# Performance work log

Hardware: AMD Instinct MI355X
Metric: run time of the kernel (lower is better)

## Reference

```python
import jax, jax.numpy as jnp
import numpy as np

B, T, D = 2, 2048, 2048
N_HEADS, N_KV = 16, 4
HD = D // N_HEADS  # 128
ROPE_BASE = 10000.0


def _rope_tables(t, dim, base=ROPE_BASE):
    inv_freq = 1.0 / (base ** (jnp.arange(0, dim, 2, dtype=jnp.float32) / dim))
    freqs = jnp.arange(t, dtype=jnp.float32)[:, None] * inv_freq[None, :]  # (T, dim/2)
    emb = jnp.concatenate([freqs, freqs], axis=-1)  # (T, dim)
    return jnp.cos(emb), jnp.sin(emb)


def _rotate_half(x):
    x1, x2 = jnp.split(x, 2, axis=-1)
    return jnp.concatenate([-x2, x1], axis=-1)


def _apply_rope(x, cos, sin):
    # x: (B, H, T, hd); cos/sin: (T, hd)
    return x * cos[None, None] + _rotate_half(x) * sin[None, None]


def setup_inputs() -> dict:
    key = jax.random.key(0)
    ks = jax.random.split(key, 5)
    s = 0.02
    return {
        "x": jax.random.normal(ks[0], (B, T, D), jnp.float32),
        "wq": jax.random.normal(ks[1], (D, N_HEADS * HD), jnp.float32) * s,
        "wk": jax.random.normal(ks[2], (D, N_KV * HD), jnp.float32) * s,
        "wv": jax.random.normal(ks[3], (D, N_KV * HD), jnp.float32) * s,
        "wo": jax.random.normal(ks[4], (D, D), jnp.float32) * s,
    }


def reference(x, wq, wk, wv, wo):
    b, t, c = x.shape
    n_rep = N_HEADS // N_KV
    scale = 1.0 / np.sqrt(HD)

    q = (x @ wq).reshape(b, t, N_HEADS, HD).transpose(0, 2, 1, 3)  # (B,H,T,hd)
    k = (x @ wk).reshape(b, t, N_KV, HD).transpose(0, 2, 1, 3)     # (B,Hkv,T,hd)
    v = (x @ wv).reshape(b, t, N_KV, HD).transpose(0, 2, 1, 3)

    cos, sin = _rope_tables(t, HD)
    q = _apply_rope(q, cos, sin)
    k = _apply_rope(k, cos, sin)

    # repeat_kv (GQA)
    k = jnp.repeat(k, n_rep, axis=1)  # (B,H,T,hd)
    v = jnp.repeat(v, n_rep, axis=1)

    scores = jnp.einsum("bhqd,bhkd->bhqk", q, k) * scale
    causal = jnp.tril(jnp.ones((t, t), dtype=bool))
    scores = jnp.where(causal[None, None], scores, -jnp.inf)
    attn = jax.nn.softmax(scores, axis=-1)
    out = jnp.einsum("bhqk,bhkd->bhqd", attn, v)
    out = out.transpose(0, 2, 1, 3).reshape(b, t, c)
    return out @ wo
```

## Files before the change

### kernel.cpp

```cpp
#include <hip/hip_runtime.h>
#include <hip/hip_bf16.h>
#include <math.h>

#define B_   2
#define T_   2048
#define D_   2048
#define NH_  16
#define NKV_ 4
#define HD_  128
#define MROWS (B_*T_)
#define NQKV  (NH_*HD_ + 2*NKV_*HD_)

typedef __bf16 bf16_t;
typedef __bf16 bf16x8 __attribute__((ext_vector_type(8)));
typedef __bf16 bf16x4 __attribute__((ext_vector_type(4)));
typedef float  floatx4 __attribute__((ext_vector_type(4)));

__device__ __forceinline__ void async_copy16(const bf16_t* gsrc, bf16_t* ldst) {
  __builtin_amdgcn_global_load_lds(
      (const __attribute__((address_space(1))) unsigned int*)gsrc,
      (__attribute__((address_space(3))) unsigned int*)ldst, 16, 0, 0);
}

__global__ void cast_f32_bf16(const float* __restrict__ src, bf16_t* __restrict__ dst, int n) {
  int i = (blockIdx.x * 256 + threadIdx.x) * 8;
  if (i >= n) return;
  float4 a = *(const float4*)(src + i);
  float4 b = *(const float4*)(src + i + 4);
  bf16x8 v;
  v[0]=(bf16_t)a.x; v[1]=(bf16_t)a.y; v[2]=(bf16_t)a.z; v[3]=(bf16_t)a.w;
  v[4]=(bf16_t)b.x; v[5]=(bf16_t)b.y; v[6]=(bf16_t)b.z; v[7]=(bf16_t)b.w;
  *(bf16x8*)(dst + i) = v;
}

__global__ void transpose_cast4(const float* __restrict__ s0, const float* __restrict__ s1,
                                const float* __restrict__ s2, const float* __restrict__ s3,
                                bf16_t* __restrict__ d0, bf16_t* __restrict__ d1,
                                bf16_t* __restrict__ d2, bf16_t* __restrict__ d3) {
  const int z = blockIdx.z;
  const int N = (z == 1 || z == 2) ? 512 : 2048;
  const int n0 = blockIdx.x * 32;
  if (n0 >= N) return;
  const float* src = (z == 0) ? s0 : (z == 1) ? s1 : (z == 2) ? s2 : s3;
  bf16_t*      dst = (z == 0) ? d0 : (z == 1) ? d1 : (z == 2) ? d2 : d3;
  const int K = 2048;
  __shared__ float tile[32][33];
  int k0 = blockIdx.y * 32;
  int tx = threadIdx.x, ty = threadIdx.y;
#pragma unroll
  for (int r = 0; r < 4; r++)
    tile[ty + r*8][tx] = src[(size_t)(k0 + ty + r*8) * N + n0 + tx];
  __syncthreads();
#pragma unroll
  for (int r = 0; r < 4; r++)
    dst[(size_t)(n0 + ty + r*8) * K + k0 + tx] = (bf16_t)tile[tx][ty + r*8];
}

template <typename OUT_T>
__global__ __launch_bounds__(256, 2)
void gemm_bt(const bf16_t* __restrict__ A, const bf16_t* __restrict__ Bt,
             OUT_T* __restrict__ C, int M, int N, int K) {
  __shared__ __align__(16) bf16_t As[128 * 64];
  __shared__ __align__(16) bf16_t Bs[128 * 64];
  const int tid  = threadIdx.x;
  const int wave = tid >> 6, lane = tid & 63;
  const int quad = lane >> 4, l16 = lane & 15;
  const int nBlocksM = M >> 7;
  const int bm = blockIdx.x % nBlocksM, bn = blockIdx.x / nBlocksM;
  const int m0 = bm * 128, n0 = bn * 128;
  const int wm = (wave >> 1) * 64, wn = (wave & 1) * 64;

  floatx4 acc[4][4];
#pragma unroll
  for (int i = 0; i < 4; i++)
#pragma unroll
    for (int j = 0; j < 4; j++) acc[i][j] = floatx4{0.f, 0.f, 0.f, 0.f};

  for (int k0 = 0; k0 < K; k0 += 64) {
    __syncthreads();
#pragma unroll
    for (int i = 0; i < 4; i++) {
      int e = i * 256 + tid;
      int row = e >> 3, grp = e & 7;
      int gg = grp ^ (row & 7);
      async_copy16(A + (size_t)(m0 + row) * K + k0 + gg * 8, As + e * 8);
    }
#pragma unroll
    for (int i = 0; i < 4; i++) {
      int e = i * 256 + tid;
      int row = e >> 3, grp = e & 7;
      int gg = grp ^ (row & 7);
      async_copy16(Bt + (size_t)(n0 + row) * K + k0 + gg * 8, Bs + e * 8);
    }
    __syncthreads();
#pragma unroll
    for (int ks = 0; ks < 2; ks++) {
      bf16x8 af[4], bfr[4];
      int grp = ks * 4 + quad;
#pragma unroll
      for (int mi = 0; mi < 4; mi++) {
        int row = wm + mi * 16 + l16;
        af[mi] = *(const bf16x8*)(As + row * 64 + ((grp ^ (row & 7)) << 3));
      }
#pragma unroll
      for (int ni = 0; ni < 4; ni++) {
        int row = wn + ni * 16 + l16;
        bfr[ni] = *(const bf16x8*)(Bs + row * 64 + ((grp ^ (row & 7)) << 3));
      }
#pragma unroll
      for (int mi = 0; mi < 4; mi++)
#pragma unroll
        for (int ni = 0; ni < 4; ni++)
          acc[mi][ni] = __builtin_amdgcn_mfma_f32_16x16x32_bf16(af[mi], bfr[ni], acc[mi][ni], 0, 0, 0);
    }
  }
#pragma unroll
  for (int mi = 0; mi < 4; mi++) {
#pragma unroll
    for (int r = 0; r < 4; r++) {
      int row = m0 + wm + mi * 16 + quad * 4 + r;
      size_t base = (size_t)row * N + n0 + wn;
#pragma unroll
      for (int ni = 0; ni < 4; ni++)
        C[base + ni * 16 + l16] = (OUT_T)acc[mi][ni][r];
    }
  }
}

__global__ void rope_scatter(const bf16_t* __restrict__ qkv,
                             bf16_t* __restrict__ Qb, bf16_t* __restrict__ Kb) {
  int g = blockIdx.x * 256 + threadIdx.x;
  int j = g & 63;
  int rest = g >> 6;
  int head = rest % (NH_ + NKV_);
  int row  = rest / (NH_ + NKV_);
  int t = row & (T_ - 1);
  int b = row >> 11;
  const bf16_t* src = qkv + (size_t)row * NQKV;
  float ang = (float)t * __expf(-0.14391156816f * (float)j);
  float sn, cs;
  __sincosf(ang, &sn, &cs);
  if (head < NH_) {
    float x0 = (float)src[head * HD_ + j];
    float x1 = (float)src[head * HD_ + 64 + j];
    const float scale = 0.12751651541057752f;
    bf16_t* dst = Qb + ((size_t)(b * NH_ + head) * T_ + t) * HD_;
    dst[j]      = (bf16_t)((x0 * cs - x1 * sn) * scale);
    dst[j + 64] = (bf16_t)((x1 * cs + x0 * sn) * scale);
  } else {
    int kvh = head - NH_;
    float x0 = (float)src[NH_ * HD_ + kvh * HD_ + j];
    float x1 = (float)src[NH_ * HD_ + kvh * HD_ + 64 + j];
    bf16_t* dst = Kb + ((size_t)(b * NKV_ + kvh) * T_ + t) * HD_;
    dst[j]      = (bf16_t)(x0 * cs - x1 * sn);
    dst[j + 64] = (bf16_t)(x1 * cs + x0 * sn);
  }
}

__global__ void v_transpose(const bf16_t* __restrict__ qkv, bf16_t* __restrict__ Vt) {
  __shared__ float tile[32][33];
  int t0 = blockIdx.x * 32, d0 = blockIdx.y * 32;
  int bk = blockIdx.z;
  int b = bk / NKV_, kvh = bk % NKV_;
  int tx = threadIdx.x, ty = threadIdx.y;
#pragma unroll
  for (int r = 0; r < 4; r++) {
    int t = t0 + ty + r * 8;
    tile[ty + r*8][tx] =
        (float)qkv[(size_t)(b * T_ + t) * NQKV + (NH_ + NKV_) * HD_ + kvh * HD_ + d0 + tx];
  }
  __syncthreads();
#pragma unroll
  for (int r = 0; r < 4; r++) {
    int d = d0 + ty + r * 8;
    Vt[((size_t)(b * NKV_ + kvh) * HD_ + d) * T_ + t0 + tx] = (bf16_t)tile[tx][ty + r*8];
  }
}

__global__ __launch_bounds__(256, 2)
void flash_attn(const bf16_t* __restrict__ Qb, const bf16_t* __restrict__ Kb,
                const bf16_t* __restrict__ Vt, bf16_t* __restrict__ Ob) {
  __shared__ __align__(16) bf16_t Ks[2][64 * 128];
  __shared__ __align__(16) bf16_t Vs[2][128 * 64];
  __shared__ __align__(16) bf16_t Ps[4][16 * 72];

  const int tid = threadIdx.x;
  const int wave = tid >> 6, lane = tid & 63;
  const int quad = lane >> 4, l16 = lane & 15;
  const int nQT = T_ / 64;
  const int bid = blockIdx.x;
  const int bh = bid % (B_ * NH_);
  const int qt = (nQT - 1) - (bid / (B_ * NH_));
  const int h = bh % NH_;
  const int b = bh / NH_;
  const int kv = h >> 2;

  const bf16_t* qbase = Qb + ((size_t)(b * NH_ + h) * T_ + qt * 64) * HD_;
  const bf16_t* kbase = Kb + ((size_t)(b * NKV_ + kv) * T_) * HD_;
  const bf16_t* vbase = Vt + ((size_t)(b * NKV_ + kv) * HD_) * T_;

  auto stage = [&](int kt, int bufi) {
#pragma unroll
    for (int i = 0; i < 4; i++) {
      int e = i * 256 + tid;
      int row = e >> 4, grp = e & 15;
      int gg = grp ^ (row & 15);
      async_copy16(kbase + (size_t)(kt * 64 + row) * HD_ + gg * 8, &Ks[bufi][e * 8]);
    }
#pragma unroll
    for (int i = 0; i < 4; i++) {
      int e = i * 256 + tid;
      int row = e >> 3, grp = e & 7;
      int gg = grp ^ (row & 7);
      async_copy16(vbase + (size_t)row * T_ + kt * 64 + gg * 8, &Vs[bufi][e * 8]);
    }
  };

  stage(0, 0);

  bf16x8 qf[4];
  {
    const bf16_t* qptr = qbase + (wave * 16 + l16) * HD_;
#pragma unroll
    for (int ks = 0; ks < 4; ks++)
      qf[ks] = *(const bf16x8*)(qptr + ks * 32 + quad * 8);
  }

  floatx4 o[8];
#pragma unroll
  for (int i = 0; i < 8; i++) o[i] = floatx4{0.f, 0.f, 0.f, 0.f};
  float m_s = -1e30f, l_s = 0.f;

  for (int kt = 0; kt <= qt; kt++) {
    const int bufi = kt & 1;
    __syncthreads();
    if (kt < qt) stage(kt + 1, bufi ^ 1);

    floatx4 s[4];
#pragma unroll
    for (int nt = 0; nt < 4; nt++) s[nt] = floatx4{0.f, 0.f, 0.f, 0.f};
#pragma unroll
    for (int ks = 0; ks < 4; ks++) {
      int grp = ks * 4 + quad;
#pragma unroll
      for (int nt = 0; nt < 4; nt++) {
        int row = nt * 16 + l16;
        bf16x8 kf = *(const bf16x8*)(&Ks[bufi][row * 128 + ((grp ^ (row & 15)) << 3)]);
        s[nt] = __builtin_amdgcn_mfma_f32_16x16x32_bf16(kf, qf[ks], s[nt], 0, 0, 0);
      }
    }

    if (kt == qt) {
      int qlocal = wave * 16 + l16;
#pragma unroll
      for (int nt = 0; nt < 4; nt++)
#pragma unroll
        for (int r = 0; r < 4; r++) {
          int klocal = nt * 16 + quad * 4 + r;
          if (klocal > qlocal) s[nt][r] = -1e30f;
        }
    }

    float mx = fmaxf(fmaxf(s[0][0], s[0][1]), fmaxf(s[0][2], s[0][3]));
#pragma unroll
    for (int nt = 1; nt < 4; nt++)
      mx = fmaxf(mx, fmaxf(fmaxf(s[nt][0], s[nt][1]), fmaxf(s[nt][2], s[nt][3])));
    mx = fmaxf(mx, __shfl_xor(mx, 16, 64));
    mx = fmaxf(mx, __shfl_xor(mx, 32, 64));
    float mnew = fmaxf(m_s, mx);
    float alpha = __builtin_amdgcn_exp2f(m_s - mnew);
    m_s = mnew;
    float sum = 0.f;
#pragma unroll
    for (int nt = 0; nt < 4; nt++)
#pragma unroll
      for (int r = 0; r < 4; r++) {
        float p = __builtin_amdgcn_exp2f(s[nt][r] - mnew);
        s[nt][r] = p;
        sum += p;
      }
    sum += __shfl_xor(sum, 16, 64);
    sum += __shfl_xor(sum, 32, 64);
    l_s = l_s * alpha + sum;
#pragma unroll
    for (int dt = 0; dt < 8; dt++) o[dt] *= alpha;

#pragma unroll
    for (int nt = 0; nt < 4; nt++) {
      bf16x4 p4;
#pragma unroll
      for (int r = 0; r < 4; r++) p4[r] = (bf16_t)s[nt][r];
      *(bf16x4*)(&Ps[wave][l16 * 72 + nt * 16 + quad * 4]) = p4;
    }

#pragma unroll
    for (int ks = 0; ks < 2; ks++) {
      bf16x8 pf = *(const bf16x8*)(&Ps[wave][l16 * 72 + ks * 32 + quad * 8]);
      int grp = ks * 4 + quad;
#pragma unroll
      for (int dt = 0; dt < 8; dt++) {
        int row = dt * 16 + l16;
        bf16x8 vf = *(const bf16x8*)(&Vs[bufi][row * 64 + ((grp ^ (row & 7)) << 3)]);
        o[dt] = __builtin_amdgcn_mfma_f32_16x16x32_bf16(vf, pf, o[dt], 0, 0, 0);
      }
    }
  }

  {
    int qg = qt * 64 + wave * 16 + l16;
    float inv_l = 1.f / l_s;
    size_t base = ((size_t)(b * T_) + qg) * D_ + h * HD_;
#pragma unroll
    for (int dt = 0; dt < 8; dt++) {
      bf16x4 w;
#pragma unroll
      for (int r = 0; r < 4; r++) w[r] = (bf16_t)(o[dt][r] * inv_l);
      *(bf16x4*)(Ob + base + dt * 16 + quad * 4) = w;
    }
  }
}

extern "C" void kernel_launch(void* const* d_in, const int* in_sizes, int n_in,
                              void* d_out, int out_size, void* d_ws, size_t ws_size,
                              hipStream_t stream) {
  const float* x  = (const float*)d_in[0];
  const float* wq = (const float*)d_in[1];
  const float* wk = (const float*)d_in[2];
  const float* wv = (const float*)d_in[3];
  const float* wo = (const float*)d_in[4];
  float* out = (float*)d_out;

  bf16_t* x_bf   = (bf16_t*)d_ws;
  bf16_t* attn_o = x_bf;
  bf16_t* wqkv_t = x_bf + (size_t)MROWS * D_;
  bf16_t* wo_t   = wqkv_t + (size_t)NQKV * D_;
  bf16_t* qkv    = wo_t + (size_t)D_ * D_;
  bf16_t* Qb     = qkv + (size_t)MROWS * NQKV;
  bf16_t* Kb     = Qb + (size_t)B_ * NH_ * T_ * HD_;
  bf16_t* Vt     = Kb + (size_t)B_ * NKV_ * T_ * HD_;

  cast_f32_bf16<<<(MROWS * D_) / (256 * 8), 256, 0, stream>>>(x, x_bf, MROWS * D_);
  transpose_cast4<<<dim3(64, 64, 4), dim3(32, 8), 0, stream>>>(
      wq, wk, wv, wo,
      wqkv_t, wqkv_t + (size_t)2048 * D_, wqkv_t + (size_t)2560 * D_, wo_t);

  gemm_bt<bf16_t><<<(MROWS / 128) * (NQKV / 128), 256, 0, stream>>>(
      x_bf, wqkv_t, qkv, MROWS, NQKV, D_);

  rope_scatter<<<(MROWS * (NH_ + NKV_) * 64) / 256, 256, 0, stream>>>(qkv, Qb, Kb);
  v_transpose<<<dim3(T_ / 32, HD_ / 32, B_ * NKV_), dim3(32, 8), 0, stream>>>(qkv, Vt);

  flash_attn<<<B_ * NH_ * (T_ / 64), 256, 0, stream>>>(Qb, Kb, Vt, attn_o);

  gemm_bt<float><<<(MROWS / 128) * (D_ / 128), 256, 0, stream>>>(
      attn_o, wo_t, out, MROWS, D_, D_);
}
```

Before: 281.7 us.

## Fuse Q RoPE into attention prologue, merge prep kernels, raise GEMM occupancy

Q rotary embedding and scaling are now computed inside the flash-attention prologue, read straight from the qkv buffer, so the separate Q scatter pass and its buffer go away and the rope kernel only handles K. The x cast and the weight transpose-casts are merged into one launch using an extra grid z-slice. The GEMM launch bound goes from 2 to 3 blocks per SIMD-group hint, which may squeeze registers. The attention prologue now does strided row loads from qkv and per-element sincos, which adds some per-block work.

```diff
diff --git a/kernel.cpp b/kernel.cpp
--- a/kernel.cpp
+++ b/kernel.cpp
@@ -22,22 +22,24 @@
       (__attribute__((address_space(3))) unsigned int*)ldst, 16, 0, 0);
 }
 
-__global__ void cast_f32_bf16(const float* __restrict__ src, bf16_t* __restrict__ dst, int n) {
-  int i = (blockIdx.x * 256 + threadIdx.x) * 8;
-  if (i >= n) return;
-  float4 a = *(const float4*)(src + i);
-  float4 b = *(const float4*)(src + i + 4);
-  bf16x8 v;
-  v[0]=(bf16_t)a.x; v[1]=(bf16_t)a.y; v[2]=(bf16_t)a.z; v[3]=(bf16_t)a.w;
-  v[4]=(bf16_t)b.x; v[5]=(bf16_t)b.y; v[6]=(bf16_t)b.z; v[7]=(bf16_t)b.w;
-  *(bf16x8*)(dst + i) = v;
-}
-
-__global__ void transpose_cast4(const float* __restrict__ s0, const float* __restrict__ s1,
-                                const float* __restrict__ s2, const float* __restrict__ s3,
-                                bf16_t* __restrict__ d0, bf16_t* __restrict__ d1,
-                                bf16_t* __restrict__ d2, bf16_t* __restrict__ d3) {
+__global__ void prep_fused(const float* __restrict__ s0, const float* __restrict__ s1,
+                           const float* __restrict__ s2, const float* __restrict__ s3,
+                           const float* __restrict__ sx,
+                           bf16_t* __restrict__ d0, bf16_t* __restrict__ d1,
+                           bf16_t* __restrict__ d2, bf16_t* __restrict__ d3,
+                           bf16_t* __restrict__ dx) {
   const int z = blockIdx.z;
+  const int tx = threadIdx.x, ty = threadIdx.y;
+  if (z == 4) {
+    int i = ((blockIdx.y * 64 + blockIdx.x) * 256 + ty * 32 + tx) * 8;
+    float4 a = *(const float4*)(sx + i);
+    float4 b = *(const float4*)(sx + i + 4);
+    bf16x8 v;
+    v[0]=(bf16_t)a.x; v[1]=(bf16_t)a.y; v[2]=(bf16_t)a.z; v[3]=(bf16_t)a.w;
+    v[4]=(bf16_t)b.x; v[5]=(bf16_t)b.y; v[6]=(bf16_t)b.z; v[7]=(bf16_t)b.w;
+    *(bf16x8*)(dx + i) = v;
+    return;
+  }
   const int N = (z == 1 || z == 2) ? 512 : 2048;
   const int n0 = blockIdx.x * 32;
   if (n0 >= N) return;
@@ -46,7 +48,6 @@
   const int K = 2048;
   __shared__ float tile[32][33];
   int k0 = blockIdx.y * 32;
-  int tx = threadIdx.x, ty = threadIdx.y;
 #pragma unroll
   for (int r = 0; r < 4; r++)
     tile[ty + r*8][tx] = src[(size_t)(k0 + ty + r*8) * N + n0 + tx];
@@ -57,7 +58,7 @@
 }
 
 template <typename OUT_T>
-__global__ __launch_bounds__(256, 2)
+__global__ __launch_bounds__(256, 3)
 void gemm_bt(const bf16_t* __restrict__ A, const bf16_t* __restrict__ Bt,
              OUT_T* __restrict__ C, int M, int N, int K) {
   __shared__ __align__(16) bf16_t As[128 * 64];
@@ -127,34 +128,23 @@
   }
 }
 
-__global__ void rope_scatter(const bf16_t* __restrict__ qkv,
-                             bf16_t* __restrict__ Qb, bf16_t* __restrict__ Kb) {
+__global__ void rope_k(const bf16_t* __restrict__ qkv, bf16_t* __restrict__ Kb) {
   int g = blockIdx.x * 256 + threadIdx.x;
   int j = g & 63;
   int rest = g >> 6;
-  int head = rest % (NH_ + NKV_);
-  int row  = rest / (NH_ + NKV_);
+  int kvh = rest & 3;
+  int row = rest >> 2;
   int t = row & (T_ - 1);
   int b = row >> 11;
-  const bf16_t* src = qkv + (size_t)row * NQKV;
+  const bf16_t* src = qkv + (size_t)row * NQKV + NH_ * HD_ + kvh * HD_;
   float ang = (float)t * __expf(-0.14391156816f * (float)j);
   float sn, cs;
   __sincosf(ang, &sn, &cs);
-  if (head < NH_) {
-    float x0 = (float)src[head * HD_ + j];
-    float x1 = (float)src[head * HD_ + 64 + j];
-    const float scale = 0.12751651541057752f;
-    bf16_t* dst = Qb + ((size_t)(b * NH_ + head) * T_ + t) * HD_;
-    dst[j]      = (bf16_t)((x0 * cs - x1 * sn) * scale);
-    dst[j + 64] = (bf16_t)((x1 * cs + x0 * sn) * scale);
-  } else {
-    int kvh = head - NH_;
-    float x0 = (float)src[NH_ * HD_ + kvh * HD_ + j];
-    float x1 = (float)src[NH_ * HD_ + kvh * HD_ + 64 + j];
-    bf16_t* dst = Kb + ((size_t)(b * NKV_ + kvh) * T_ + t) * HD_;
-    dst[j]      = (bf16_t)(x0 * cs - x1 * sn);
-    dst[j + 64] = (bf16_t)(x1 * cs + x0 * sn);
-  }
+  float x0 = (float)src[j];
+  float x1 = (float)src[j + 64];
+  bf16_t* dst = Kb + ((size_t)(b * NKV_ + kvh) * T_ + t) * HD_;
+  dst[j]      = (bf16_t)(x0 * cs - x1 * sn);
+  dst[j + 64] = (bf16_t)(x1 * cs + x0 * sn);
 }
 
 __global__ void v_transpose(const bf16_t* __restrict__ qkv, bf16_t* __restrict__ Vt) {
@@ -178,7 +168,7 @@
 }
 
 __global__ __launch_bounds__(256, 2)
-void flash_attn(const bf16_t* __restrict__ Qb, const bf16_t* __restrict__ Kb,
+void flash_attn(const bf16_t* __restrict__ qkv, const bf16_t* __restrict__ Kb,
                 const bf16_t* __restrict__ Vt, bf16_t* __restrict__ Ob) {
   __shared__ __align__(16) bf16_t Ks[2][64 * 128];
   __shared__ __align__(16) bf16_t Vs[2][128 * 64];
@@ -195,7 +185,6 @@
   const int b = bh / NH_;
   const int kv = h >> 2;
 
-  const bf16_t* qbase = Qb + ((size_t)(b * NH_ + h) * T_ + qt * 64) * HD_;
   const bf16_t* kbase = Kb + ((size_t)(b * NKV_ + kv) * T_) * HD_;
   const bf16_t* vbase = Vt + ((size_t)(b * NKV_ + kv) * HD_) * T_;
 
@@ -220,10 +209,25 @@
 
   bf16x8 qf[4];
   {
-    const bf16_t* qptr = qbase + (wave * 16 + l16) * HD_;
+    const int t_row = qt * 64 + wave * 16 + l16;
+    const bf16_t* qptr = qkv + (size_t)(b * T_ + t_row) * NQKV + h * HD_;
+    bf16x8 qraw[4];
 #pragma unroll
     for (int ks = 0; ks < 4; ks++)
-      qf[ks] = *(const bf16x8*)(qptr + ks * 32 + quad * 8);
+      qraw[ks] = *(const bf16x8*)(qptr + ks * 32 + quad * 8);
+    const float scale = 0.12751651541057752f;
+#pragma unroll
+    for (int ks = 0; ks < 2; ks++)
+#pragma unroll
+      for (int j = 0; j < 8; j++) {
+        int d = ks * 32 + quad * 8 + j;
+        float ang = (float)t_row * __expf(-0.14391156816f * (float)d);
+        float sn, cs;
+        __sincosf(ang, &sn, &cs);
+        float lo = (float)qraw[ks][j], hi = (float)qraw[ks + 2][j];
+        qf[ks][j]     = (bf16_t)((lo * cs - hi * sn) * scale);
+        qf[ks + 2][j] = (bf16_t)((hi * cs + lo * sn) * scale);
+      }
   }
 
   floatx4 o[8];
@@ -335,22 +339,20 @@
   bf16_t* wqkv_t = x_bf + (size_t)MROWS * D_;
   bf16_t* wo_t   = wqkv_t + (size_t)NQKV * D_;
   bf16_t* qkv    = wo_t + (size_t)D_ * D_;
-  bf16_t* Qb     = qkv + (size_t)MROWS * NQKV;
-  bf16_t* Kb     = Qb + (size_t)B_ * NH_ * T_ * HD_;
+  bf16_t* Kb     = qkv + (size_t)MROWS * NQKV;
   bf16_t* Vt     = Kb + (size_t)B_ * NKV_ * T_ * HD_;
 
-  cast_f32_bf16<<<(MROWS * D_) / (256 * 8), 256, 0, stream>>>(x, x_bf, MROWS * D_);
-  transpose_cast4<<<dim3(64, 64, 4), dim3(32, 8), 0, stream>>>(
-      wq, wk, wv, wo,
-      wqkv_t, wqkv_t + (size_t)2048 * D_, wqkv_t + (size_t)2560 * D_, wo_t);
+  prep_fused<<<dim3(64, 64, 5), dim3(32, 8), 0, stream>>>(
+      wq, wk, wv, wo, x,
+      wqkv_t, wqkv_t + (size_t)2048 * D_, wqkv_t + (size_t)2560 * D_, wo_t, x_bf);
 
   gemm_bt<bf16_t><<<(MROWS / 128) * (NQKV / 128), 256, 0, stream>>>(
       x_bf, wqkv_t, qkv, MROWS, NQKV, D_);
 
-  rope_scatter<<<(MROWS * (NH_ + NKV_) * 64) / 256, 256, 0, stream>>>(qkv, Qb, Kb);
+  rope_k<<<(MROWS * NKV_ * 64) / 256, 256, 0, stream>>>(qkv, Kb);
   v_transpose<<<dim3(T_ / 32, HD_ / 32, B_ * NKV_), dim3(32, 8), 0, stream>>>(qkv, Vt);
 
-  flash_attn<<<B_ * NH_ * (T_ / 64), 256, 0, stream>>>(Qb, Kb, Vt, attn_o);
+  flash_attn<<<B_ * NH_ * (T_ / 64), 256, 0, stream>>>(qkv, Kb, Vt, attn_o);
 
   gemm_bt<float><<<(MROWS / 128) * (D_ / 128), 256, 0, stream>>>(
       attn_o, wo_t, out, MROWS, D_, D_);
```

Measured after the change: 264.7 us. 6.0% less time.
